# Optimization experiments

Measured on AMD Instinct MI355X. Metric: run time of the kernel, lower is better.

## Reference

```python
import jax, jax.numpy as jnp
import numpy as np

EMBED = 256
HEADS = 8
LEVELS = 1
POINTS = 4
NBQ = 2          # num_bev_queue
HBEV = 128
WBEV = 128
BS = 1


def setup_inputs() -> dict:
    key = jax.random.key(0)
    ks = jax.random.split(key, 10)
    Nq = HBEV * WBEV
    E = EMBED
    so_out = NBQ * HEADS * LEVELS * POINTS * 2
    aw_out = NBQ * HEADS * LEVELS * POINTS
    return {
        "query": jax.random.normal(ks[0], (BS, Nq, E), jnp.float32),
        "value": jax.random.normal(ks[1], (BS, NBQ * Nq, E), jnp.float32),
        "reference_points": jax.random.uniform(ks[2], (BS, Nq, LEVELS, 2), jnp.float32),
        # params stored as [in, out]; y = x @ W + b (math-equivalent to torch Linear)
        "W_vproj": jax.random.normal(ks[3], (E, E), jnp.float32) / np.sqrt(E).astype(np.float32),
        "b_vproj": jnp.zeros((E,), jnp.float32),
        "W_so": jax.random.normal(ks[4], (NBQ * E, so_out), jnp.float32) * 0.01,
        "b_so": jax.random.normal(ks[5], (so_out,), jnp.float32) * 0.5,
        "W_aw": jax.random.normal(ks[6], (NBQ * E, aw_out), jnp.float32) * 0.01,
        "b_aw": jnp.zeros((aw_out,), jnp.float32),
        "W_out": jax.random.normal(ks[7], (E, E), jnp.float32) / np.sqrt(E).astype(np.float32),
        "b_out": jnp.zeros((E,), jnp.float32),
        "spatial_shapes": jnp.array([[HBEV, WBEV]], jnp.int32),
        "level_start_index": jnp.array([0], jnp.int32),
    }


def _msda(value, spatial_shapes, sampling_locations, attention_weights):
    """Multi-scale deformable attention (grid_sample semantics: bilinear,
    zero padding, align_corners=False).
    value: [B, sum(H*W), Hh, d]; sampling_locations: [B, Nq, Hh, L, P, 2] in [0,1];
    attention_weights: [B, Nq, Hh, L, P]. Returns [B, Nq, Hh*d]."""
    B, _, Hh, d = value.shape
    _, Nq, _, L, P, _ = sampling_locations.shape
    ss = np.asarray(spatial_shapes)
    out = jnp.zeros((B, Nq, Hh, d), value.dtype)
    start = 0
    for l in range(L):
        H_, W_ = int(ss[l, 0]), int(ss[l, 1])
        v = value[:, start:start + H_ * W_]          # [B, H*W, Hh, d]
        start += H_ * W_
        loc = sampling_locations[:, :, :, l]          # [B, Nq, Hh, P, 2]
        # align_corners=False: pixel = loc*size - 0.5
        px = loc[..., 0] * W_ - 0.5
        py = loc[..., 1] * H_ - 0.5
        x0f = jnp.floor(px)
        y0f = jnp.floor(py)
        lx = px - x0f
        ly = py - y0f
        x0 = x0f.astype(jnp.int32)
        y0 = y0f.astype(jnp.int32)

        def gather(ix, iy):
            valid = ((ix >= 0) & (ix < W_) & (iy >= 0) & (iy < H_))
            idx = jnp.clip(iy, 0, H_ - 1) * W_ + jnp.clip(ix, 0, W_ - 1)   # [B,Nq,Hh,P]
            idx = jnp.transpose(idx, (0, 1, 3, 2)).reshape(B, Nq * P, Hh, 1)
            g = jnp.take_along_axis(v, idx, axis=1).reshape(B, Nq, P, Hh, d)
            m = jnp.transpose(valid, (0, 1, 3, 2))[..., None].astype(value.dtype)
            return g * m

        def wmul(w):  # [B,Nq,Hh,P] -> [B,Nq,P,Hh,1]
            return jnp.transpose(w, (0, 1, 3, 2))[..., None]

        sampled = (wmul((1 - lx) * (1 - ly)) * gather(x0, y0)
                   + wmul(lx * (1 - ly)) * gather(x0 + 1, y0)
                   + wmul((1 - lx) * ly) * gather(x0, y0 + 1)
                   + wmul(lx * ly) * gather(x0 + 1, y0 + 1))   # [B,Nq,P,Hh,d]
        out = out + jnp.einsum('bqphd,bqhp->bqhd', sampled, attention_weights[:, :, :, l])
    return out.reshape(B, Nq, Hh * d)


def reference(query, value, reference_points, W_vproj, b_vproj, W_so, b_so,
              W_aw, b_aw, W_out, b_out, spatial_shapes, level_start_index):
    bs, Nq, E = query.shape
    Hh, L, P, nbq = HEADS, LEVELS, POINTS, NBQ
    identity = query
    # query enhanced with the previous-BEV slice of value
    qe = jnp.concatenate([value[:, :Nq], query], axis=-1)        # [bs, Nq, 2E]
    v = (value @ W_vproj + b_vproj).reshape(bs * nbq, Nq, Hh, E // Hh)
    so = (qe @ W_so + b_so).reshape(bs, Nq, Hh, nbq, L, P, 2)
    aw = jax.nn.softmax((qe @ W_aw + b_aw).reshape(bs, Nq, Hh, nbq, L * P), axis=-1)
    aw = aw.reshape(bs, Nq, Hh, nbq, L, P)
    aw = jnp.transpose(aw, (0, 3, 1, 2, 4, 5)).reshape(bs * nbq, Nq, Hh, L, P)
    so = jnp.transpose(so, (0, 3, 1, 2, 4, 5, 6)).reshape(bs * nbq, Nq, Hh, L, P, 2)
    rp = jnp.tile(reference_points, (nbq, 1, 1, 1))              # [bs*nbq, Nq, L, 2]
    ssf = spatial_shapes.astype(so.dtype)
    offset_normalizer = jnp.stack([ssf[:, 1], ssf[:, 0]], -1)    # [L, 2] = (W, H)
    loc = rp[:, :, None, :, None, :] + so / offset_normalizer[None, None, None, :, None, :]
    out = _msda(v, spatial_shapes, loc, aw).reshape(bs, nbq, Nq, E).mean(axis=1)
    out = out @ W_out + b_out
    return out + identity  # dropout is identity in eval mode
```

## Files before the change

kernel.cpp:

```cpp
#include <hip/hip_runtime.h>
#include <math.h>

#define NQ     16384
#define NHEAD  8
#define GW     128
#define GH     128

typedef __attribute__((ext_vector_type(8))) short short8;
typedef __attribute__((ext_vector_type(4))) float f32x4;

static __device__ __forceinline__ unsigned short f2bf(float f) {
    unsigned u = __builtin_bit_cast(unsigned, f);
    u += 0x7FFFu + ((u >> 16) & 1u);
    return (unsigned short)(u >> 16);
}
static __device__ __forceinline__ unsigned pk2(float lo, float hi) {
    return (unsigned)f2bf(lo) | ((unsigned)f2bf(hi) << 16);
}
static __device__ __forceinline__ float bflo(unsigned u) {
    return __builtin_bit_cast(float, u << 16);
}
static __device__ __forceinline__ float bfhi(unsigned u) {
    return __builtin_bit_cast(float, u & 0xffff0000u);
}

__global__ void prep(const float* __restrict__ Wv, const float* __restrict__ Wso,
                     const float* __restrict__ Waw, const float* __restrict__ bso,
                     const float* __restrict__ baw, const float* __restrict__ Wo,
                     unsigned short* __restrict__ WTv, unsigned short* __restrict__ WTso,
                     unsigned short* __restrict__ WTo, float* __restrict__ bias2)
{
    const int n = blockIdx.x;
    const int k = threadIdx.x;
    WTv[n * 256 + k] = f2bf(Wv[(size_t)k * 256 + n]);
    WTo[n * 256 + k] = f2bf(Wo[(size_t)k * 256 + n]);
    float s0, s1;
    if (n < 128)      { s0 = Wso[(size_t)k * 128 + n];       s1 = Wso[(size_t)(k + 256) * 128 + n]; }
    else if (n < 192) { s0 = Waw[(size_t)k * 64 + n - 128];  s1 = Waw[(size_t)(k + 256) * 64 + n - 128]; }
    else              { s0 = 0.f; s1 = 0.f; }
    WTso[(size_t)n * 512 + k]       = f2bf(s0);
    WTso[(size_t)n * 512 + k + 256] = f2bf(s1);
    if (k == 0) bias2[n] = (n < 128) ? bso[n] : ((n < 192) ? baw[n - 128] : 0.f);
}

template<int KTOT, int MODE>
static __device__ __forceinline__ void gemm_body(
    int m0, int n0,
    const float* __restrict__ A1, const float* __restrict__ A2,
    const unsigned short* __restrict__ Abf,
    const unsigned short* __restrict__ WT,
    const float* __restrict__ bias, const float* __restrict__ resid,
    void* __restrict__ Cout,
    unsigned short* As, unsigned short* Bs)
{
    const int tid = threadIdx.x;
    const int w = tid >> 6, lane = tid & 63;
    const int wr = w >> 1, wc = w & 1;
    const int g = lane >> 4, r16 = lane & 15;
    const int arow = tid >> 3, aoc = tid & 7;
    const int NT = KTOT / 64;

    float4 ra[4];
    uint4  rab[2];
    uint4  rb[4];
    f32x4 acc[2][4] = {};

#define LOAD_T(t)                                                               \
    {                                                                           \
        int k0 = (t) * 64;                                                      \
        if (MODE == 2) {                                                        \
            _Pragma("unroll")                                                   \
            for (int i = 0; i < 2; ++i)                                         \
                rab[i] = *(const uint4*)&Abf[(size_t)(m0 + arow + i * 32) * 256 \
                                             + k0 + aoc * 8];                   \
        } else {                                                                \
            const float* Asrc = (KTOT == 512 && k0 >= 256) ? (A2 + (k0 - 256))  \
                                                           : (A1 + k0);         \
            _Pragma("unroll")                                                   \
            for (int i = 0; i < 2; ++i) {                                       \
                const float* p = Asrc + (size_t)(m0 + arow + i * 32) * 256      \
                                 + aoc * 8;                                     \
                ra[i * 2 + 0] = *(const float4*)p;                              \
                ra[i * 2 + 1] = *(const float4*)(p + 4);                        \
            }                                                                   \
        }                                                                       \
        _Pragma("unroll")                                                       \
        for (int i = 0; i < 4; ++i)                                             \
            rb[i] = *(const uint4*)&WT[(size_t)(n0 + arow + i * 32) * KTOT      \
                                       + k0 + aoc * 8];                         \
    }

#define WRITE_T(bufi)                                                           \
    {                                                                           \
        unsigned short* Ab = As + (bufi) * 64 * 64;                             \
        unsigned short* Bb = Bs + (bufi) * 128 * 64;                            \
        if (MODE == 2) {                                                        \
            _Pragma("unroll")                                                   \
            for (int i = 0; i < 2; ++i)                                         \
                *(uint4*)&Ab[(arow + i * 32) * 64 + aoc * 8] = rab[i];          \
        } else {                                                                \
            _Pragma("unroll")                                                   \
            for (int i = 0; i < 2; ++i) {                                       \
                uint4 wv;                                                       \
                wv.x = pk2(ra[i * 2].x, ra[i * 2].y);                           \
                wv.y = pk2(ra[i * 2].z, ra[i * 2].w);                           \
                wv.z = pk2(ra[i * 2 + 1].x, ra[i * 2 + 1].y);                   \
                wv.w = pk2(ra[i * 2 + 1].z, ra[i * 2 + 1].w);                   \
                *(uint4*)&Ab[(arow + i * 32) * 64 + aoc * 8] = wv;              \
            }                                                                   \
        }                                                                       \
        _Pragma("unroll")                                                       \
        for (int i = 0; i < 4; ++i)                                             \
            *(uint4*)&Bb[(arow + i * 32) * 64 + aoc * 8] = rb[i];               \
    }

    LOAD_T(0);
    WRITE_T(0);
    __syncthreads();

    for (int t = 0; t < NT; ++t) {
        if (t + 1 < NT) LOAD_T(t + 1);
        const unsigned short* Ab = As + (t & 1) * 64 * 64;
        const unsigned short* Bb = Bs + (t & 1) * 128 * 64;
        #pragma unroll
        for (int kh = 0; kh < 2; ++kh) {
            short8 af[2], bfr[4];
            #pragma unroll
            for (int mi = 0; mi < 2; ++mi)
                af[mi] = *(const short8*)&Ab[(wr * 32 + mi * 16 + r16) * 64
                                             + (kh * 4 + g) * 8];
            #pragma unroll
            for (int nj = 0; nj < 4; ++nj)
                bfr[nj] = *(const short8*)&Bb[(wc * 64 + nj * 16 + r16) * 64
                                              + (kh * 4 + g) * 8];
            #pragma unroll
            for (int mi = 0; mi < 2; ++mi)
                #pragma unroll
                for (int nj = 0; nj < 4; ++nj)
                    acc[mi][nj] = __builtin_amdgcn_mfma_f32_16x16x32_bf16(
                        af[mi], bfr[nj], acc[mi][nj], 0, 0, 0);
        }
        if (t + 1 < NT) WRITE_T((t + 1) & 1);
        __syncthreads();
    }
#undef LOAD_T
#undef WRITE_T

    #pragma unroll
    for (int mi = 0; mi < 2; ++mi) {
        int row = m0 + wr * 32 + mi * 16 + g * 4;
        #pragma unroll
        for (int nj = 0; nj < 4; ++nj) {
            int col = n0 + wc * 64 + nj * 16 + r16;
            if (MODE == 1 && col >= 192) continue;
            float bia = bias[col];
            #pragma unroll
            for (int j = 0; j < 4; ++j) {
                float vo = acc[mi][nj][j] + bia;
                if (MODE == 0) {
                    ((unsigned short*)Cout)[(size_t)(row + j) * 256 + col] = f2bf(vo);
                } else if (MODE == 1) {
                    ((float*)Cout)[(size_t)(row + j) * 192 + col] = vo;
                } else {
                    ((float*)Cout)[(size_t)(row + j) * 256 + col] =
                        vo + resid[(size_t)(row + j) * 256 + col];
                }
            }
        }
    }
}

__global__ __launch_bounds__(256)
void gemm_vproj(const float* __restrict__ value, const unsigned short* __restrict__ WTv,
                const float* __restrict__ bv, unsigned short* __restrict__ v_out)
{
    __shared__ __align__(16) unsigned short As[2 * 64 * 64];
    __shared__ __align__(16) unsigned short Bs[2 * 128 * 64];
    gemm_body<256, 0>((blockIdx.x >> 1) * 64, (blockIdx.x & 1) * 128,
                      value, nullptr, nullptr, WTv, bv, nullptr, v_out, As, Bs);
}

__global__ __launch_bounds__(256)
void gemm_soaw(const float* __restrict__ value, const float* __restrict__ query,
               const unsigned short* __restrict__ WTso, const float* __restrict__ bias2,
               float* __restrict__ soaw_out)
{
    __shared__ __align__(16) unsigned short As[2 * 64 * 64];
    __shared__ __align__(16) unsigned short Bs[2 * 128 * 64];
    gemm_body<512, 1>((blockIdx.x >> 1) * 64, (blockIdx.x & 1) * 128,
                      value, query, nullptr, WTso, bias2, nullptr, soaw_out, As, Bs);
}

__global__ __launch_bounds__(256)
void gemm_out(const unsigned short* __restrict__ Abf, const unsigned short* __restrict__ WTo,
              const float* __restrict__ bo, const float* __restrict__ resid,
              float* __restrict__ out)
{
    __shared__ __align__(16) unsigned short As[2 * 64 * 64];
    __shared__ __align__(16) unsigned short Bs[2 * 128 * 64];
    gemm_body<256, 2>((blockIdx.x >> 1) * 64, (blockIdx.x & 1) * 128,
                      nullptr, nullptr, Abf, WTo, bo, resid, out, As, Bs);
}

static __device__ __forceinline__ void acc8(float* acc, float w, uint4 r) {
    acc[0] = fmaf(w, bflo(r.x), acc[0]);
    acc[1] = fmaf(w, bfhi(r.x), acc[1]);
    acc[2] = fmaf(w, bflo(r.y), acc[2]);
    acc[3] = fmaf(w, bfhi(r.y), acc[3]);
    acc[4] = fmaf(w, bflo(r.z), acc[4]);
    acc[5] = fmaf(w, bfhi(r.z), acc[5]);
    acc[6] = fmaf(w, bflo(r.w), acc[6]);
    acc[7] = fmaf(w, bfhi(r.w), acc[7]);
}

__global__ __launch_bounds__(256)
void sampler(const unsigned short* __restrict__ v, const float* __restrict__ soaw,
             const float* __restrict__ rp, unsigned short* __restrict__ outm)
{
    __shared__ float so_s[8][128];
    __shared__ float w_s[8][64];
    __shared__ float rp_s[8][2];

    const int t = threadIdx.x;
    const int bid = blockIdx.x;
    const int q0 = ((bid & 7) * 256 + (bid >> 3)) * 8;

    #pragma unroll
    for (int i = 0; i < 4; ++i) {
        int idx = t + i * 256;
        int qq = idx >> 7, off = idx & 127;
        so_s[qq][off] = soaw[(size_t)(q0 + qq) * 192 + off];
    }
    if (t < 128) {
        int qq = t >> 4, grp = t & 15;
        float4 a4 = *reinterpret_cast<const float4*>(
            &soaw[(size_t)(q0 + qq) * 192 + 128 + grp * 4]);
        float m = fmaxf(fmaxf(a4.x, a4.y), fmaxf(a4.z, a4.w));
        float e0 = __expf(a4.x - m), e1 = __expf(a4.y - m);
        float e2 = __expf(a4.z - m), e3 = __expf(a4.w - m);
        float inv = 1.f / (e0 + e1 + e2 + e3);
        w_s[qq][grp * 4 + 0] = e0 * inv;
        w_s[qq][grp * 4 + 1] = e1 * inv;
        w_s[qq][grp * 4 + 2] = e2 * inv;
        w_s[qq][grp * 4 + 3] = e3 * inv;
    }
    if (t < 16) rp_s[t >> 1][t & 1] = rp[(size_t)(q0 + (t >> 1)) * 2 + (t & 1)];
    __syncthreads();

    const int wq = t >> 5;
    const int q = q0 + wq;
    const int s = t & 31;
    const int h = s >> 2, c = s & 3;
    const int sub = h * 64 + c * 16;
    const float rpx = rp_s[wq][0], rpy = rp_s[wq][1];
    float acc[8] = {};

    #pragma unroll
    for (int b = 0; b < 2; ++b) {
        const char* vb = (const char*)v + (size_t)b * NQ * 512;
        #pragma unroll
        for (int p = 0; p < 4; ++p) {
            float sox = so_s[wq][h * 16 + b * 8 + p * 2 + 0];
            float soy = so_s[wq][h * 16 + b * 8 + p * 2 + 1];
            float wbp = w_s[wq][h * 8 + b * 4 + p];
            float px = (rpx + sox * (1.0f / 128.0f)) * 128.0f - 0.5f;
            float py = (rpy + soy * (1.0f / 128.0f)) * 128.0f - 0.5f;
            float x0f = floorf(px), y0f = floorf(py);
            float lx = px - x0f, ly = py - y0f;
            int x0 = (int)x0f, y0 = (int)y0f;
            int x1 = x0 + 1, y1 = y0 + 1;
            float wx0 = (1.f - lx) * ((x0 >= 0 && x0 < GW) ? 1.f : 0.f);
            float wx1 = lx         * ((x1 >= 0 && x1 < GW) ? 1.f : 0.f);
            float wy0 = (1.f - ly) * ((y0 >= 0 && y0 < GH) ? 1.f : 0.f);
            float wy1 = ly         * ((y1 >= 0 && y1 < GH) ? 1.f : 0.f);
            int x0c = min(max(x0, 0), GW - 1), x1c = min(max(x1, 0), GW - 1);
            int y0c = min(max(y0, 0), GH - 1), y1c = min(max(y1, 0), GH - 1);
            uint4 r00 = *(const uint4*)(vb + ((size_t)(y0c * GW + x0c) * 512 + sub));
            uint4 r10 = *(const uint4*)(vb + ((size_t)(y0c * GW + x1c) * 512 + sub));
            uint4 r01 = *(const uint4*)(vb + ((size_t)(y1c * GW + x0c) * 512 + sub));
            uint4 r11 = *(const uint4*)(vb + ((size_t)(y1c * GW + x1c) * 512 + sub));
            acc8(acc, wbp * wx0 * wy0, r00);
            acc8(acc, wbp * wx1 * wy0, r10);
            acc8(acc, wbp * wx0 * wy1, r01);
            acc8(acc, wbp * wx1 * wy1, r11);
        }
    }

    uint4 o;
    o.x = pk2(0.5f * acc[0], 0.5f * acc[1]);
    o.y = pk2(0.5f * acc[2], 0.5f * acc[3]);
    o.z = pk2(0.5f * acc[4], 0.5f * acc[5]);
    o.w = pk2(0.5f * acc[6], 0.5f * acc[7]);
    *reinterpret_cast<uint4*>((char*)outm + (size_t)q * 512 + sub) = o;
}

extern "C" void kernel_launch(void* const* d_in, const int* in_sizes, int n_in,
                              void* d_out, int out_size, void* d_ws, size_t ws_size,
                              hipStream_t stream)
{
    const float* query   = (const float*)d_in[0];
    const float* value   = (const float*)d_in[1];
    const float* rp      = (const float*)d_in[2];
    const float* W_vproj = (const float*)d_in[3];
    const float* b_vproj = (const float*)d_in[4];
    const float* W_so    = (const float*)d_in[5];
    const float* b_so    = (const float*)d_in[6];
    const float* W_aw    = (const float*)d_in[7];
    const float* b_aw    = (const float*)d_in[8];
    const float* W_out   = (const float*)d_in[9];
    const float* b_out   = (const float*)d_in[10];
    float* out = (float*)d_out;

    char* wp = (char*)d_ws;
    unsigned short* ws_v    = (unsigned short*)wp; wp += (size_t)2 * NQ * 256 * 2;
    float*          ws_soaw = (float*)wp;          wp += (size_t)NQ * 192 * 4;
    unsigned short* ws_mean = (unsigned short*)wp; wp += (size_t)NQ * 256 * 2;
    unsigned short* WTv     = (unsigned short*)wp; wp += 256 * 256 * 2;
    unsigned short* WTso    = (unsigned short*)wp; wp += 256 * 512 * 2;
    unsigned short* WTo     = (unsigned short*)wp; wp += 256 * 256 * 2;
    float*          bias2   = (float*)wp;          wp += 256 * 4;

    prep<<<dim3(256), dim3(256), 0, stream>>>(W_vproj, W_so, W_aw, b_so, b_aw, W_out,
                                              WTv, WTso, WTo, bias2);
    gemm_vproj<<<dim3(1024), dim3(256), 0, stream>>>(value, WTv, b_vproj, ws_v);
    gemm_soaw<<<dim3(512), dim3(256), 0, stream>>>(value, query, WTso, bias2, ws_soaw);
    sampler<<<dim3(NQ / 8), dim3(256), 0, stream>>>(ws_v, ws_soaw, rp, ws_mean);
    gemm_out<<<dim3(512), dim3(256), 0, stream>>>(ws_mean, WTo, b_out, query, out);
}
```

Measured before the change: 83.30 us.

## Merge vproj and soaw GEMMs into one launch; split sampler by BEV queue

```diff
diff --git a/kernel.cpp b/kernel.cpp
--- a/kernel.cpp
+++ b/kernel.cpp
@@ -171,24 +171,22 @@
 }
 
 __global__ __launch_bounds__(256)
-void gemm_vproj(const float* __restrict__ value, const unsigned short* __restrict__ WTv,
-                const float* __restrict__ bv, unsigned short* __restrict__ v_out)
+void gemm_vs(const float* __restrict__ value, const float* __restrict__ query,
+             const unsigned short* __restrict__ WTv, const unsigned short* __restrict__ WTso,
+             const float* __restrict__ bv, const float* __restrict__ bias2,
+             unsigned short* __restrict__ v_out, float* __restrict__ soaw_out)
 {
     __shared__ __align__(16) unsigned short As[2 * 64 * 64];
     __shared__ __align__(16) unsigned short Bs[2 * 128 * 64];
-    gemm_body<256, 0>((blockIdx.x >> 1) * 64, (blockIdx.x & 1) * 128,
-                      value, nullptr, nullptr, WTv, bv, nullptr, v_out, As, Bs);
-}
-
-__global__ __launch_bounds__(256)
-void gemm_soaw(const float* __restrict__ value, const float* __restrict__ query,
-               const unsigned short* __restrict__ WTso, const float* __restrict__ bias2,
-               float* __restrict__ soaw_out)
-{
-    __shared__ __align__(16) unsigned short As[2 * 64 * 64];
-    __shared__ __align__(16) unsigned short Bs[2 * 128 * 64];
-    gemm_body<512, 1>((blockIdx.x >> 1) * 64, (blockIdx.x & 1) * 128,
-                      value, query, nullptr, WTso, bias2, nullptr, soaw_out, As, Bs);
+    const int bid = blockIdx.x;
+    if (bid < 1024) {
+        gemm_body<256, 0>((bid >> 1) * 64, (bid & 1) * 128,
+                          value, nullptr, nullptr, WTv, bv, nullptr, v_out, As, Bs);
+    } else {
+        const int b2 = bid - 1024;
+        gemm_body<512, 1>((b2 >> 1) * 64, (b2 & 1) * 128,
+                          value, query, nullptr, WTso, bias2, nullptr, soaw_out, As, Bs);
+    }
 }
 
 __global__ __launch_bounds__(256)
@@ -217,21 +215,21 @@
 void sampler(const unsigned short* __restrict__ v, const float* __restrict__ soaw,
              const float* __restrict__ rp, unsigned short* __restrict__ outm)
 {
-    __shared__ float so_s[8][128];
-    __shared__ float w_s[8][64];
-    __shared__ float rp_s[8][2];
+    __shared__ float so_s[4][128];
+    __shared__ float w_s[4][64];
+    __shared__ float rp_s[4][2];
 
     const int t = threadIdx.x;
     const int bid = blockIdx.x;
-    const int q0 = ((bid & 7) * 256 + (bid >> 3)) * 8;
+    const int q0 = ((bid & 7) * 512 + (bid >> 3)) * 4;
 
     #pragma unroll
-    for (int i = 0; i < 4; ++i) {
+    for (int i = 0; i < 2; ++i) {
         int idx = t + i * 256;
         int qq = idx >> 7, off = idx & 127;
         so_s[qq][off] = soaw[(size_t)(q0 + qq) * 192 + off];
     }
-    if (t < 128) {
+    if (t < 64) {
         int qq = t >> 4, grp = t & 15;
         float4 a4 = *reinterpret_cast<const float4*>(
             &soaw[(size_t)(q0 + qq) * 192 + 128 + grp * 4]);
@@ -244,54 +242,58 @@
         w_s[qq][grp * 4 + 2] = e2 * inv;
         w_s[qq][grp * 4 + 3] = e3 * inv;
     }
-    if (t < 16) rp_s[t >> 1][t & 1] = rp[(size_t)(q0 + (t >> 1)) * 2 + (t & 1)];
+    if (t < 8) rp_s[t >> 1][t & 1] = rp[(size_t)(q0 + (t >> 1)) * 2 + (t & 1)];
     __syncthreads();
 
-    const int wq = t >> 5;
+    const int wq = t >> 6;
     const int q = q0 + wq;
-    const int s = t & 31;
+    const int ln = t & 63;
+    const int b = ln >> 5;
+    const int s = ln & 31;
     const int h = s >> 2, c = s & 3;
     const int sub = h * 64 + c * 16;
     const float rpx = rp_s[wq][0], rpy = rp_s[wq][1];
+    const char* vb = (const char*)v + (size_t)b * NQ * 512;
     float acc[8] = {};
 
     #pragma unroll
-    for (int b = 0; b < 2; ++b) {
-        const char* vb = (const char*)v + (size_t)b * NQ * 512;
-        #pragma unroll
-        for (int p = 0; p < 4; ++p) {
-            float sox = so_s[wq][h * 16 + b * 8 + p * 2 + 0];
-            float soy = so_s[wq][h * 16 + b * 8 + p * 2 + 1];
-            float wbp = w_s[wq][h * 8 + b * 4 + p];
-            float px = (rpx + sox * (1.0f / 128.0f)) * 128.0f - 0.5f;
-            float py = (rpy + soy * (1.0f / 128.0f)) * 128.0f - 0.5f;
-            float x0f = floorf(px), y0f = floorf(py);
-            float lx = px - x0f, ly = py - y0f;
-            int x0 = (int)x0f, y0 = (int)y0f;
-            int x1 = x0 + 1, y1 = y0 + 1;
-            float wx0 = (1.f - lx) * ((x0 >= 0 && x0 < GW) ? 1.f : 0.f);
-            float wx1 = lx         * ((x1 >= 0 && x1 < GW) ? 1.f : 0.f);
-            float wy0 = (1.f - ly) * ((y0 >= 0 && y0 < GH) ? 1.f : 0.f);
-            float wy1 = ly         * ((y1 >= 0 && y1 < GH) ? 1.f : 0.f);
-            int x0c = min(max(x0, 0), GW - 1), x1c = min(max(x1, 0), GW - 1);
-            int y0c = min(max(y0, 0), GH - 1), y1c = min(max(y1, 0), GH - 1);
-            uint4 r00 = *(const uint4*)(vb + ((size_t)(y0c * GW + x0c) * 512 + sub));
-            uint4 r10 = *(const uint4*)(vb + ((size_t)(y0c * GW + x1c) * 512 + sub));
-            uint4 r01 = *(const uint4*)(vb + ((size_t)(y1c * GW + x0c) * 512 + sub));
-            uint4 r11 = *(const uint4*)(vb + ((size_t)(y1c * GW + x1c) * 512 + sub));
-            acc8(acc, wbp * wx0 * wy0, r00);
-            acc8(acc, wbp * wx1 * wy0, r10);
-            acc8(acc, wbp * wx0 * wy1, r01);
-            acc8(acc, wbp * wx1 * wy1, r11);
-        }
-    }
-
-    uint4 o;
-    o.x = pk2(0.5f * acc[0], 0.5f * acc[1]);
-    o.y = pk2(0.5f * acc[2], 0.5f * acc[3]);
-    o.z = pk2(0.5f * acc[4], 0.5f * acc[5]);
-    o.w = pk2(0.5f * acc[6], 0.5f * acc[7]);
-    *reinterpret_cast<uint4*>((char*)outm + (size_t)q * 512 + sub) = o;
+    for (int p = 0; p < 4; ++p) {
+        float sox = so_s[wq][h * 16 + b * 8 + p * 2 + 0];
+        float soy = so_s[wq][h * 16 + b * 8 + p * 2 + 1];
+        float wbp = w_s[wq][h * 8 + b * 4 + p];
+        float px = (rpx + sox * (1.0f / 128.0f)) * 128.0f - 0.5f;
+        float py = (rpy + soy * (1.0f / 128.0f)) * 128.0f - 0.5f;
+        float x0f = floorf(px), y0f = floorf(py);
+        float lx = px - x0f, ly = py - y0f;
+        int x0 = (int)x0f, y0 = (int)y0f;
+        int x1 = x0 + 1, y1 = y0 + 1;
+        float wx0 = (1.f - lx) * ((x0 >= 0 && x0 < GW) ? 1.f : 0.f);
+        float wx1 = lx         * ((x1 >= 0 && x1 < GW) ? 1.f : 0.f);
+        float wy0 = (1.f - ly) * ((y0 >= 0 && y0 < GH) ? 1.f : 0.f);
+        float wy1 = ly         * ((y1 >= 0 && y1 < GH) ? 1.f : 0.f);
+        int x0c = min(max(x0, 0), GW - 1), x1c = min(max(x1, 0), GW - 1);
+        int y0c = min(max(y0, 0), GH - 1), y1c = min(max(y1, 0), GH - 1);
+        uint4 r00 = *(const uint4*)(vb + ((size_t)(y0c * GW + x0c) * 512 + sub));
+        uint4 r10 = *(const uint4*)(vb + ((size_t)(y0c * GW + x1c) * 512 + sub));
+        uint4 r01 = *(const uint4*)(vb + ((size_t)(y1c * GW + x0c) * 512 + sub));
+        uint4 r11 = *(const uint4*)(vb + ((size_t)(y1c * GW + x1c) * 512 + sub));
+        acc8(acc, wbp * wx0 * wy0, r00);
+        acc8(acc, wbp * wx1 * wy0, r10);
+        acc8(acc, wbp * wx0 * wy1, r01);
+        acc8(acc, wbp * wx1 * wy1, r11);
+    }
+
+    #pragma unroll
+    for (int i = 0; i < 8; ++i) acc[i] += __shfl_xor(acc[i], 32);
+
+    if (b == 0) {
+        uint4 o;
+        o.x = pk2(0.5f * acc[0], 0.5f * acc[1]);
+        o.y = pk2(0.5f * acc[2], 0.5f * acc[3]);
+        o.z = pk2(0.5f * acc[4], 0.5f * acc[5]);
+        o.w = pk2(0.5f * acc[6], 0.5f * acc[7]);
+        *reinterpret_cast<uint4*>((char*)outm + (size_t)q * 512 + sub) = o;
+    }
 }
 
 extern "C" void kernel_launch(void* const* d_in, const int* in_sizes, int n_in,
@@ -322,8 +324,8 @@
 
     prep<<<dim3(256), dim3(256), 0, stream>>>(W_vproj, W_so, W_aw, b_so, b_aw, W_out,
                                               WTv, WTso, WTo, bias2);
-    gemm_vproj<<<dim3(1024), dim3(256), 0, stream>>>(value, WTv, b_vproj, ws_v);
-    gemm_soaw<<<dim3(512), dim3(256), 0, stream>>>(value, query, WTso, bias2, ws_soaw);
-    sampler<<<dim3(NQ / 8), dim3(256), 0, stream>>>(ws_v, ws_soaw, rp, ws_mean);
+    gemm_vs<<<dim3(1536), dim3(256), 0, stream>>>(value, query, WTv, WTso,
+                                                  b_vproj, bias2, ws_v, ws_soaw);
+    sampler<<<dim3(NQ / 4), dim3(256), 0, stream>>>(ws_v, ws_soaw, rp, ws_mean);
     gemm_out<<<dim3(512), dim3(256), 0, stream>>>(ws_mean, WTo, b_out, query, out);
 }
```

Result: no change. 83.53 us (+0.3%).
